# Optimization experiments

Hardware: AMD Instinct MI355X
Metric: run time of the kernel (lower is better)

## Reference

```python
import jax, jax.numpy as jnp
import numpy as np

N = 8192
DIN = 128
DOUT = 128
EPS = 1e-7
GAMMA_MAX = 1e7


def _mobius_scalar_mul(r, x):
    # Moebius scalar multiplication on the Poincare ball (c=1):
    # r (.) x = tanh(r * arctanh(||x||)) * x / ||x||
    n = jnp.linalg.norm(x, axis=-1, keepdims=True)
    n_safe = jnp.clip(n, EPS, 1.0 - EPS)
    return jnp.tanh(r * jnp.arctanh(n_safe)) * x / n_safe


def _logmap0(x):
    n = jnp.linalg.norm(x, axis=-1, keepdims=True)
    n_safe = jnp.clip(n, EPS, 1.0 - EPS)
    return jnp.arctanh(n_safe) * x / n_safe


def _expmap0(v):
    n = jnp.linalg.norm(v, axis=-1, keepdims=True)
    n_safe = jnp.maximum(n, EPS)
    return jnp.tanh(n_safe) * v / n_safe


def setup_inputs() -> dict:
    key = jax.random.key(0)
    k1, k2, k3, k4 = jax.random.split(key, 4)
    # node features inside the Poincare ball (small norm)
    x = 0.01 * jax.random.normal(k1, (N, DIN), dtype=jnp.float32)
    # sparse-ish binary adjacency stored dense (module treats adj as dense [N,N])
    adj = (jax.random.uniform(k2, (N, N)) < 0.004).astype(jnp.float32)
    W = 0.05 * jax.random.normal(k3, (DIN, DOUT), dtype=jnp.float32)
    b = 0.05 * jax.random.normal(k4, (DOUT,), dtype=jnp.float32)
    return {"x": x, "adj": adj, "W": W, "b": b}


def reference(x, adj, W, b):
    n = adj.shape[0]
    # adj <- I + adj, then symmetric degree normalization D^{-1/2} A D^{-1/2}
    a = jnp.eye(n, dtype=adj.dtype) + adj
    D = 1.0 / jnp.sqrt(jnp.sum(a, axis=1))
    a = a * D[:, None] * D[None, :]
    # gyromidpoint-style weighted aggregation (gamma broadcast over rows, as in torch)
    r2 = jnp.sum(x * x, axis=-1, keepdims=True)            # [N,1]
    gamma = jnp.minimum(2.0 / (1.0 - r2), GAMMA_MAX)        # [N,1]
    num = a * gamma                                          # [N,N]
    den = jnp.sum(a * (gamma - 1.0), axis=-1, keepdims=True)  # [N,1]
    coef = num / den                                         # [N,N]
    aggr = coef @ x                                          # [N,DIN]
    aggr = _mobius_scalar_mul(0.5, aggr)
    # PoincareFC: logmap0 -> linear -> act -> expmap0 (to_tan=False)
    u = _logmap0(aggr)
    y = jax.nn.relu(u @ W + b)
    return _expmap0(y)
```

## Files before the change

kernel.cpp:

```cpp
#include <hip/hip_runtime.h>
#include <cstdint>
#include <cstddef>

#define N_NODES 8192
#define DIN 128
#define DOUT 128
#define CAP 128
#define EPSF 1e-7f

typedef unsigned short u16;

__global__ __launch_bounds__(256) void k_build(const float4* __restrict__ adj,
                                               u16* __restrict__ cols,
                                               int* __restrict__ counts) {
    const int lane = threadIdx.x & 63;
    const int row  = blockIdx.x * 4 + (threadIdx.x >> 6);
    const float4* rp = adj + (size_t)row * (N_NODES / 4);
    u16* cl = cols + (size_t)row * CAP;
    const unsigned long long lt_mask = (1ULL << lane) - 1ULL;

    int base = 0;
    for (int it = 0; it < N_NODES / 256; ++it) {
        float4 v = rp[it * 64 + lane];
        int cb = it * 256 + lane * 4;
        {
            bool nz = (v.x != 0.0f);
            unsigned long long m = __ballot(nz);
            if (nz) { int p = base + __popcll(m & lt_mask); if (p < CAP) cl[p] = (u16)(cb + 0); }
            base += __popcll(m);
        }
        {
            bool nz = (v.y != 0.0f);
            unsigned long long m = __ballot(nz);
            if (nz) { int p = base + __popcll(m & lt_mask); if (p < CAP) cl[p] = (u16)(cb + 1); }
            base += __popcll(m);
        }
        {
            bool nz = (v.z != 0.0f);
            unsigned long long m = __ballot(nz);
            if (nz) { int p = base + __popcll(m & lt_mask); if (p < CAP) cl[p] = (u16)(cb + 2); }
            base += __popcll(m);
        }
        {
            bool nz = (v.w != 0.0f);
            unsigned long long m = __ballot(nz);
            if (nz) { int p = base + __popcll(m & lt_mask); if (p < CAP) cl[p] = (u16)(cb + 3); }
            base += __popcll(m);
        }
    }
    if (lane == 0) counts[row] = base;
}

__global__ void k_deg(const int* __restrict__ counts, float* __restrict__ Dv) {
    int i = blockIdx.x * blockDim.x + threadIdx.x;
    Dv[i] = 1.0f / sqrtf(1.0f + (float)counts[i]);
}

__device__ inline float blockSum128(float v, volatile float* red, int tid) {
#pragma unroll
    for (int m = 32; m >= 1; m >>= 1) v += __shfl_xor(v, m, 64);
    __syncthreads();
    if ((tid & 63) == 0) red[tid >> 6] = v;
    __syncthreads();
    return red[0] + red[1];
}

__global__ __launch_bounds__(128) void k_agg(const float* __restrict__ x,
                                             const float* __restrict__ Dv,
                                             const u16* __restrict__ cols,
                                             const int* __restrict__ counts,
                                             float* __restrict__ u) {
    __shared__ u16   colsL[CAP];
    __shared__ float djL[CAP];
    __shared__ float red[2];

    const int row = blockIdx.x;
    const int d   = threadIdx.x;
    int c = counts[row];
    if (c > CAP) c = CAP;

    colsL[d] = cols[(size_t)row * CAP + d];
    __syncthreads();
    djL[d] = (d < c) ? Dv[colsL[d]] : 0.0f;
    const float xi = x[(size_t)row * DIN + d];
    const float Di = Dv[row];
    __syncthreads();

    float acc  = Di * xi;
    float sumw = Di;
#pragma unroll 4
    for (int k = 0; k < c; ++k) {
        int   j  = colsL[k];
        float dj = djL[k];
        sumw += dj;
        acc = fmaf(dj, x[(size_t)j * DIN + d], acc);
    }

    float r2 = blockSum128(xi * xi, red, d);
    float gamma = fminf(2.0f / (1.0f - r2), 1e7f);
    float ag = (gamma / ((gamma - 1.0f) * sumw)) * acc;

    float n2 = blockSum128(ag * ag, red, d);
    float n  = sqrtf(n2);
    float nsafe = fminf(fmaxf(n, EPSF), 1.0f - EPSF);
    float t  = tanhf(0.5f * atanhf(nsafe));
    float nm = t * (n / nsafe);
    float nmsafe = fminf(fmaxf(nm, EPSF), 1.0f - EPSF);
    float ud = (atanhf(nmsafe) / nmsafe) * (t / nsafe) * ag;

    u[(size_t)row * DIN + d] = ud;
}

__global__ __launch_bounds__(256) void k_fc(const float* __restrict__ u,
                                            const float* __restrict__ W,
                                            const float* __restrict__ b,
                                            float* __restrict__ out) {
    __shared__ float4 WL4[DIN * 32];
    const int tid = threadIdx.x;
    const float4* W4 = (const float4*)W;
    for (int i = tid; i < DIN * 32; i += 256) WL4[i] = W4[i];

    const int og = tid & 31;
    const int rg = tid >> 5;
    const float4 bv = ((const float4*)b)[og];
    __syncthreads();

    const int row_base = blockIdx.x * 16;
    for (int chunk = 0; chunk < 16; chunk += 8) {
        const int row = row_base + chunk + rg;
        float4 uv = ((const float4*)u)[(size_t)row * 32 + og];
        float a0 = bv.x, a1 = bv.y, a2 = bv.z, a3 = bv.w;
#pragma unroll 8
        for (int q = 0; q < 32; ++q) {
            float u0 = __shfl(uv.x, q, 32);
            float u1 = __shfl(uv.y, q, 32);
            float u2 = __shfl(uv.z, q, 32);
            float u3 = __shfl(uv.w, q, 32);
            float4 w0 = WL4[(4 * q + 0) * 32 + og];
            float4 w1 = WL4[(4 * q + 1) * 32 + og];
            float4 w2 = WL4[(4 * q + 2) * 32 + og];
            float4 w3 = WL4[(4 * q + 3) * 32 + og];
            a0 = fmaf(u0, w0.x, fmaf(u1, w1.x, fmaf(u2, w2.x, fmaf(u3, w3.x, a0))));
            a1 = fmaf(u0, w0.y, fmaf(u1, w1.y, fmaf(u2, w2.y, fmaf(u3, w3.y, a1))));
            a2 = fmaf(u0, w0.z, fmaf(u1, w1.z, fmaf(u2, w2.z, fmaf(u3, w3.z, a2))));
            a3 = fmaf(u0, w0.w, fmaf(u1, w1.w, fmaf(u2, w2.w, fmaf(u3, w3.w, a3))));
        }
        a0 = fmaxf(a0, 0.0f); a1 = fmaxf(a1, 0.0f);
        a2 = fmaxf(a2, 0.0f); a3 = fmaxf(a3, 0.0f);
        float ss = fmaf(a0, a0, fmaf(a1, a1, fmaf(a2, a2, a3 * a3)));
#pragma unroll
        for (int m = 16; m >= 1; m >>= 1) ss += __shfl_xor(ss, m, 32);
        float ny = sqrtf(ss);
        float ns = fmaxf(ny, EPSF);
        float sc = tanhf(ns) / ns;
        float4 o;
        o.x = a0 * sc; o.y = a1 * sc; o.z = a2 * sc; o.w = a3 * sc;
        ((float4*)out)[(size_t)row * 32 + og] = o;
    }
}

extern "C" void kernel_launch(void* const* d_in, const int* in_sizes, int n_in,
                              void* d_out, int out_size, void* d_ws, size_t ws_size,
                              hipStream_t stream) {
    const float* x   = (const float*)d_in[0];
    const float* adj = (const float*)d_in[1];
    const float* W   = (const float*)d_in[2];
    const float* b   = (const float*)d_in[3];
    float* out = (float*)d_out;

    char* ws = (char*)d_ws;
    int*   counts = (int*)ws;
    float* Dv     = (float*)(ws + 32768);
    u16*   cols   = (u16*)(ws + 65536);
    float* u      = (float*)(ws + 65536 + (size_t)N_NODES * CAP * 2);

    hipLaunchKernelGGL(k_build, dim3(N_NODES / 4), dim3(256), 0, stream,
                       (const float4*)adj, cols, counts);
    hipLaunchKernelGGL(k_deg, dim3(N_NODES / 256), dim3(256), 0, stream,
                       counts, Dv);
    hipLaunchKernelGGL(k_agg, dim3(N_NODES), dim3(128), 0, stream,
                       x, Dv, cols, counts, u);
    hipLaunchKernelGGL(k_fc, dim3(N_NODES / 16), dim3(256), 0, stream,
                       u, W, b, out);
}
```

Measured before the change: 407.1 us.

## Fuse degree normalization into build and aggregation with FC into one kernel

The degree-to-normalization computation moves into the adjacency compaction kernel, removing the separate k_deg launch. The aggregation and Poincaré FC stages merge into one kernel that processes four rows per block, keeping the intermediate u in shared memory instead of writing it to and reading it back from global memory. The FC step now reads W straight from global or cache in every block rather than staging it in LDS. The compaction loop also gets a 2x unroll hint. The dominant cost, the scan of the dense adjacency matrix, is unchanged.

```diff
diff --git a/kernel.cpp b/kernel.cpp
--- a/kernel.cpp
+++ b/kernel.cpp
@@ -4,15 +4,16 @@
 
 #define N_NODES 8192
 #define DIN 128
-#define DOUT 128
 #define CAP 128
 #define EPSF 1e-7f
+#define RPB 4
 
 typedef unsigned short u16;
 
 __global__ __launch_bounds__(256) void k_build(const float4* __restrict__ adj,
                                                u16* __restrict__ cols,
-                                               int* __restrict__ counts) {
+                                               int* __restrict__ counts,
+                                               float* __restrict__ Dv) {
     const int lane = threadIdx.x & 63;
     const int row  = blockIdx.x * 4 + (threadIdx.x >> 6);
     const float4* rp = adj + (size_t)row * (N_NODES / 4);
@@ -20,6 +21,7 @@
     const unsigned long long lt_mask = (1ULL << lane) - 1ULL;
 
     int base = 0;
+#pragma unroll 2
     for (int it = 0; it < N_NODES / 256; ++it) {
         float4 v = rp[it * 64 + lane];
         int cb = it * 256 + lane * 4;
@@ -48,15 +50,13 @@
             base += __popcll(m);
         }
     }
-    if (lane == 0) counts[row] = base;
+    if (lane == 0) {
+        counts[row] = base;
+        Dv[row] = 1.0f / sqrtf(1.0f + (float)base);
+    }
 }
 
-__global__ void k_deg(const int* __restrict__ counts, float* __restrict__ Dv) {
-    int i = blockIdx.x * blockDim.x + threadIdx.x;
-    Dv[i] = 1.0f / sqrtf(1.0f + (float)counts[i]);
-}
-
-__device__ inline float blockSum128(float v, volatile float* red, int tid) {
+__device__ __forceinline__ float blockSum128(float v, volatile float* red, int tid) {
 #pragma unroll
     for (int m = 32; m >= 1; m >>= 1) v += __shfl_xor(v, m, 64);
     __syncthreads();
@@ -65,97 +65,75 @@
     return red[0] + red[1];
 }
 
-__global__ __launch_bounds__(128) void k_agg(const float* __restrict__ x,
-                                             const float* __restrict__ Dv,
-                                             const u16* __restrict__ cols,
-                                             const int* __restrict__ counts,
-                                             float* __restrict__ u) {
+__global__ __launch_bounds__(128) void k_fused(const float* __restrict__ x,
+                                               const float* __restrict__ Dv,
+                                               const u16* __restrict__ cols,
+                                               const int* __restrict__ counts,
+                                               const float* __restrict__ W,
+                                               const float* __restrict__ b,
+                                               float* __restrict__ out) {
     __shared__ u16   colsL[CAP];
     __shared__ float djL[CAP];
     __shared__ float red[2];
+    __shared__ float uL[RPB][DIN];
 
-    const int row = blockIdx.x;
-    const int d   = threadIdx.x;
-    int c = counts[row];
-    if (c > CAP) c = CAP;
+    const int d    = threadIdx.x;
+    const int row0 = blockIdx.x * RPB;
 
-    colsL[d] = cols[(size_t)row * CAP + d];
-    __syncthreads();
-    djL[d] = (d < c) ? Dv[colsL[d]] : 0.0f;
-    const float xi = x[(size_t)row * DIN + d];
-    const float Di = Dv[row];
+    for (int r = 0; r < RPB; ++r) {
+        const int row = row0 + r;
+        int c = counts[row];
+        if (c > CAP) c = CAP;
+        colsL[d] = cols[(size_t)row * CAP + d];
+        const float xi = x[(size_t)row * DIN + d];
+        const float Di = Dv[row];
+        djL[d] = (d < c) ? Dv[colsL[d]] : 0.0f;
+        __syncthreads();
+
+        float acc  = Di * xi;
+        float sumw = Di;
+#pragma unroll 4
+        for (int k = 0; k < c; ++k) {
+            int   j  = colsL[k];
+            float dj = djL[k];
+            sumw += dj;
+            acc = fmaf(dj, x[(size_t)j * DIN + d], acc);
+        }
+
+        float r2 = blockSum128(xi * xi, red, d);
+        float gamma = fminf(2.0f / (1.0f - r2), 1e7f);
+        float ag = (gamma / ((gamma - 1.0f) * sumw)) * acc;
+
+        float n2 = blockSum128(ag * ag, red, d);
+        float n  = sqrtf(n2);
+        float nsafe = fminf(fmaxf(n, EPSF), 1.0f - EPSF);
+        float t  = tanhf(0.5f * atanhf(nsafe));
+        float nm = t * (n / nsafe);
+        float nmsafe = fminf(fmaxf(nm, EPSF), 1.0f - EPSF);
+        uL[r][d] = (atanhf(nmsafe) / nmsafe) * (t / nsafe) * ag;
+    }
     __syncthreads();
 
-    float acc  = Di * xi;
-    float sumw = Di;
+    float av[RPB];
+#pragma unroll
+    for (int r = 0; r < RPB; ++r) av[r] = b[d];
+    const float* Wc = W + d;
 #pragma unroll 4
-    for (int k = 0; k < c; ++k) {
-        int   j  = colsL[k];
-        float dj = djL[k];
-        sumw += dj;
-        acc = fmaf(dj, x[(size_t)j * DIN + d], acc);
+    for (int k = 0; k < DIN; ++k) {
+        float wkd = Wc[(size_t)k * DIN];
+#pragma unroll
+        for (int r = 0; r < RPB; ++r)
+            av[r] = fmaf(uL[r][k], wkd, av[r]);
     }
 
-    float r2 = blockSum128(xi * xi, red, d);
-    float gamma = fminf(2.0f / (1.0f - r2), 1e7f);
-    float ag = (gamma / ((gamma - 1.0f) * sumw)) * acc;
-
-    float n2 = blockSum128(ag * ag, red, d);
-    float n  = sqrtf(n2);
-    float nsafe = fminf(fmaxf(n, EPSF), 1.0f - EPSF);
-    float t  = tanhf(0.5f * atanhf(nsafe));
-    float nm = t * (n / nsafe);
-    float nmsafe = fminf(fmaxf(nm, EPSF), 1.0f - EPSF);
-    float ud = (atanhf(nmsafe) / nmsafe) * (t / nsafe) * ag;
-
-    u[(size_t)row * DIN + d] = ud;
-}
-
-__global__ __launch_bounds__(256) void k_fc(const float* __restrict__ u,
-                                            const float* __restrict__ W,
-                                            const float* __restrict__ b,
-                                            float* __restrict__ out) {
-    __shared__ float4 WL4[DIN * 32];
-    const int tid = threadIdx.x;
-    const float4* W4 = (const float4*)W;
-    for (int i = tid; i < DIN * 32; i += 256) WL4[i] = W4[i];
-
-    const int og = tid & 31;
-    const int rg = tid >> 5;
-    const float4 bv = ((const float4*)b)[og];
-    __syncthreads();
-
-    const int row_base = blockIdx.x * 16;
-    for (int chunk = 0; chunk < 16; chunk += 8) {
-        const int row = row_base + chunk + rg;
-        float4 uv = ((const float4*)u)[(size_t)row * 32 + og];
-        float a0 = bv.x, a1 = bv.y, a2 = bv.z, a3 = bv.w;
-#pragma unroll 8
-        for (int q = 0; q < 32; ++q) {
-            float u0 = __shfl(uv.x, q, 32);
-            float u1 = __shfl(uv.y, q, 32);
-            float u2 = __shfl(uv.z, q, 32);
-            float u3 = __shfl(uv.w, q, 32);
-            float4 w0 = WL4[(4 * q + 0) * 32 + og];
-            float4 w1 = WL4[(4 * q + 1) * 32 + og];
-            float4 w2 = WL4[(4 * q + 2) * 32 + og];
-            float4 w3 = WL4[(4 * q + 3) * 32 + og];
-            a0 = fmaf(u0, w0.x, fmaf(u1, w1.x, fmaf(u2, w2.x, fmaf(u3, w3.x, a0))));
-            a1 = fmaf(u0, w0.y, fmaf(u1, w1.y, fmaf(u2, w2.y, fmaf(u3, w3.y, a1))));
-            a2 = fmaf(u0, w0.z, fmaf(u1, w1.z, fmaf(u2, w2.z, fmaf(u3, w3.z, a2))));
-            a3 = fmaf(u0, w0.w, fmaf(u1, w1.w, fmaf(u2, w2.w, fmaf(u3, w3.w, a3))));
-        }
-        a0 = fmaxf(a0, 0.0f); a1 = fmaxf(a1, 0.0f);
-        a2 = fmaxf(a2, 0.0f); a3 = fmaxf(a3, 0.0f);
-        float ss = fmaf(a0, a0, fmaf(a1, a1, fmaf(a2, a2, a3 * a3)));
 #pragma unroll
-        for (int m = 16; m >= 1; m >>= 1) ss += __shfl_xor(ss, m, 32);
+    for (int r = 0; r < RPB; ++r) {
+        float y  = fmaxf(av[r], 0.0f);
+        float ss = blockSum128(y * y, red, d);
         float ny = sqrtf(ss);
         float ns = fmaxf(ny, EPSF);
         float sc = tanhf(ns) / ns;
-        float4 o;
-        o.x = a0 * sc; o.y = a1 * sc; o.z = a2 * sc; o.w = a3 * sc;
-        ((float4*)out)[(size_t)row * 32 + og] = o;
+        out[(size_t)(row0 + r) * DIN + d] = y * sc;
     }
 }
 
@@ -172,14 +150,9 @@
     int*   counts = (int*)ws;
     float* Dv     = (float*)(ws + 32768);
     u16*   cols   = (u16*)(ws + 65536);
-    float* u      = (float*)(ws + 65536 + (size_t)N_NODES * CAP * 2);
 
     hipLaunchKernelGGL(k_build, dim3(N_NODES / 4), dim3(256), 0, stream,
-                       (const float4*)adj, cols, counts);
-    hipLaunchKernelGGL(k_deg, dim3(N_NODES / 256), dim3(256), 0, stream,
-                       counts, Dv);
-    hipLaunchKernelGGL(k_agg, dim3(N_NODES), dim3(128), 0, stream,
-                       x, Dv, cols, counts, u);
-    hipLaunchKernelGGL(k_fc, dim3(N_NODES / 16), dim3(256), 0, stream,
-                       u, W, b, out);
+                       (const float4*)adj, cols, counts, Dv);
+    hipLaunchKernelGGL(k_fused, dim3(N_NODES / RPB), dim3(128), 0, stream,
+                       x, Dv, cols, counts, W, b, out);
 }
```

After: 403.5 us. No clear change (-0.9%).
